# Kernel optimization log

Measured on AMD Instinct MI355X. Metric: run time of the kernel, lower is better.

## Reference

```python
import jax, jax.numpy as jnp
import numpy as np

N_NODES = 100000
N_EDGES = 1600000
D_IN = 64
D_OUT = 64


def setup_inputs() -> dict:
    key = jax.random.key(0)
    k1, k2, k3, k4, k5 = jax.random.split(key, 5)
    feat = jax.random.normal(k1, (N_NODES, D_IN), dtype=jnp.float32)
    src = jax.random.randint(k2, (N_EDGES,), 0, N_NODES, dtype=jnp.int64)
    dst = jax.random.randint(k3, (N_EDGES,), 0, N_NODES, dtype=jnp.int64)
    # Xavier-uniform init with relu gain, as in reset_parameters()
    gain = np.sqrt(2.0)
    bound = gain * np.sqrt(6.0 / (D_IN + D_OUT))
    W_self = jax.random.uniform(k4, (D_OUT, D_IN), minval=-bound, maxval=bound, dtype=jnp.float32)
    W_neigh = jax.random.uniform(k5, (D_OUT, D_IN), minval=-bound, maxval=bound, dtype=jnp.float32)
    return {"feat": feat, "src": src, "dst": dst, "W_self": W_self, "W_neigh": W_neigh}


def _spmm_mean(feat, src, dst, n_nodes):
    # Mean neighbor aggregation: for each dst node, average src features.
    gathered = feat[src]  # [E, D] irregular gather
    agg = jax.ops.segment_sum(gathered, dst, num_segments=n_nodes)  # [N, D]
    deg = jax.ops.segment_sum(jnp.ones((src.shape[0],), feat.dtype), dst, num_segments=n_nodes)
    return agg / jnp.maximum(deg, 1.0)[:, None]


def reference(feat, src, dst, W_self, W_neigh):
    neigh = _spmm_mean(feat, src, dst, feat.shape[0])  # [N, D_in]
    # rst = fc_self(feat) + fc_neigh(SpMM(feat))
    return feat @ W_self.T + neigh @ W_neigh.T
```

## Files before the change

kernel.cpp:

```cpp
#include <hip/hip_runtime.h>
#include <hip/hip_fp16.h>

#define N_NODES 100000
#define N_EDGES 1600000
#define D 64
#define ZROW 100000

#define NPB   240
#define NB    417
#define CAP   8192

#define EPB   8192
#define PBLK  ((N_EDGES + EPB - 1) / EPB)

#define W2_FF16     0u
#define W2_PACKED   12800128u
#define W2_CNT      (W2_PACKED + 4u * N_EDGES)
#define W2_OFF      (W2_CNT  + 4u * NB)
#define W2_GCUR     (W2_OFF  + 4u * NB)
#define W2_NODEOFF  (W2_GCUR + 4u * NB)
#define W2_NODECNT  (W2_NODEOFF + 4u * N_NODES)
#define W2_W16      (W2_NODECNT + 4u * N_NODES)
#define W2_NEED     (W2_W16 + 16384u)

#define W1_PACKED   0u
#define W1_CNT      (4u * N_EDGES)
#define W1_OFF      (W1_CNT  + 4u * NB)
#define W1_GCUR     (W1_OFF  + 4u * NB)
#define W1_NODEOFF  (W1_GCUR + 4u * NB)
#define W1_NODECNT  (W1_NODEOFF + 4u * N_NODES)
#define W1_NEED     (W1_NODECNT + 4u * N_NODES)

typedef __attribute__((ext_vector_type(8))) _Float16 half8;
typedef __attribute__((ext_vector_type(4))) float f32x4;

__device__ inline unsigned int h2bits(__half2 h) { return *(unsigned int*)&h; }
__device__ inline __half2 bits2h(unsigned int u) { return *(__half2*)&u; }
__device__ inline __half2 h2shfl_xor(__half2 x, int mask) {
    int i = *(int*)&x;
    i = __shfl_xor(i, mask);
    return *(__half2*)&i;
}

__global__ __launch_bounds__(256) void k_prep(
    const float* __restrict__ feat, const int* __restrict__ dst,
    const float* __restrict__ Ws, const float* __restrict__ Wn,
    unsigned int* __restrict__ ff16, int* __restrict__ cnt,
    unsigned int* __restrict__ w16)
{
    __shared__ int h[NB];
    const int bid = blockIdx.x;
    const int t   = threadIdx.x;

    if (bid < 1024) {
        const int total = N_NODES * D / 8;
        for (int i = bid * 256 + t; i < total; i += 1024 * 256) {
            const float4 x = ((const float4*)feat)[i * 2];
            const float4 y = ((const float4*)feat)[i * 2 + 1];
            uint4 o;
            o.x = h2bits(__floats2half2_rn(x.x, x.y));
            o.y = h2bits(__floats2half2_rn(x.z, x.w));
            o.z = h2bits(__floats2half2_rn(y.x, y.y));
            o.w = h2bits(__floats2half2_rn(y.z, y.w));
            ((uint4*)ff16)[i] = o;
        }
    } else if (bid < 1280) {
        for (int i = t; i < NB; i += 256) h[i] = 0;
        __syncthreads();
        for (int e = (bid - 1024) * 256 + t; e < N_EDGES; e += 256 * 256)
            atomicAdd(&h[dst[e] / NPB], 1);
        __syncthreads();
        for (int i = t; i < NB; i += 256)
            if (h[i]) atomicAdd(&cnt[i], h[i]);
    } else {
        for (int i = t; i < 2048; i += 256)
            w16[i] = h2bits(__floats2half2_rn(Ws[2 * i], Ws[2 * i + 1]));
        for (int i = t; i < 2048; i += 256)
            w16[2048 + i] = h2bits(__floats2half2_rn(Wn[2 * i], Wn[2 * i + 1]));
        if (t < 32) ff16[ZROW * 32 + t] = 0;
    }
}

__global__ __launch_bounds__(512) void k_scan(
    const int* __restrict__ cnt, int* __restrict__ off, int* __restrict__ gcur)
{
    __shared__ int lds[512];
    const int t = threadIdx.x;
    const int v = (t < NB) ? cnt[t] : 0;
    lds[t] = v;
    __syncthreads();
    for (int o = 1; o < 512; o <<= 1) {
        const int x = (t >= o) ? lds[t - o] : 0;
        __syncthreads();
        lds[t] += x;
        __syncthreads();
    }
    if (t < NB) {
        const int excl = lds[t] - v;
        off[t]  = excl;
        gcur[t] = excl;
    }
}

__global__ __launch_bounds__(1024) void k_partition(
    const int* __restrict__ src, const int* __restrict__ dst,
    int* __restrict__ gcur, int* __restrict__ packed)
{
    __shared__ int recs[EPB];
    __shared__ int cnt[NB];
    __shared__ int scn[512];
    __shared__ int pos[NB];
    __shared__ int cur[NB];
    __shared__ int dlt[NB];

    const int t  = threadIdx.x;
    const int e0 = blockIdx.x * EPB;
    const int nE = min(EPB, N_EDGES - e0);

    for (int i = t; i < NB; i += 1024) cnt[i] = 0;
    __syncthreads();

    int pk[8], bk[8];
    #pragma unroll
    for (int k = 0; k < 8; ++k) {
        const int i = t + k * 1024;
        if (i < nE) {
            const int d  = dst[e0 + i];
            const int b  = d / NPB;
            const int dl = d - b * NPB;
            pk[k] = src[e0 + i] | (dl << 17);
            bk[k] = b;
            atomicAdd(&cnt[b], 1);
        } else {
            bk[k] = -1;
        }
    }
    __syncthreads();

    if (t < 512) scn[t] = (t < NB) ? cnt[t] : 0;
    __syncthreads();
    for (int o = 1; o < 512; o <<= 1) {
        int x = 0;
        if (t < 512 && t >= o) x = scn[t - o];
        __syncthreads();
        if (t < 512) scn[t] += x;
        __syncthreads();
    }
    if (t < NB) {
        const int v    = cnt[t];
        const int excl = scn[t] - v;
        pos[t] = excl;
        cur[t] = excl;
        dlt[t] = atomicAdd(&gcur[t], v);
    }
    __syncthreads();

    #pragma unroll
    for (int k = 0; k < 8; ++k) {
        if (bk[k] >= 0) {
            const int p = atomicAdd(&cur[bk[k]], 1);
            recs[p] = pk[k];
        }
    }
    __syncthreads();

    const int w    = t >> 6;
    const int lane = t & 63;
    for (int b = w; b < NB; b += 16) {
        const int n = cnt[b];
        const int o = pos[b];
        const int g = dlt[b];
        for (int i = lane; i < n; i += 64)
            packed[g + i] = recs[o + i];
    }
}

__global__ __launch_bounds__(512) void k_sortb(
    const int* __restrict__ off, const int* __restrict__ cntg,
    int* packed,
    int* __restrict__ node_off, int* __restrict__ node_cnt)
{
    __shared__ int recs[CAP];
    __shared__ int lcnt[256];
    __shared__ int sc[256];
    __shared__ int lcur[NPB];

    const int t      = threadIdx.x;
    const int bucket = blockIdx.x;
    const int base   = off[bucket];
    int total = cntg[bucket];
    if (total > CAP) total = CAP;

    if (t < 256) lcnt[t] = 0;
    __syncthreads();

    for (int i = t; i < total; i += 512) {
        const int r = packed[base + i];
        recs[i] = r;
        atomicAdd(&lcnt[r >> 17], 1);
    }
    __syncthreads();

    if (t < 256) sc[t] = lcnt[t];
    __syncthreads();
    for (int o = 1; o < 256; o <<= 1) {
        int x = 0;
        if (t < 256 && t >= o) x = sc[t - o];
        __syncthreads();
        if (t < 256) sc[t] += x;
        __syncthreads();
    }

    if (t < NPB) {
        const int excl = sc[t] - lcnt[t];
        lcur[t] = excl;
        const int n = bucket * NPB + t;
        if (n < N_NODES) {
            node_off[n] = base + excl;
            node_cnt[n] = lcnt[t];
        }
    }
    __syncthreads();

    for (int i = t; i < total; i += 512) {
        const int r   = recs[i];
        const int pos = atomicAdd(&lcur[r >> 17], 1);
        packed[base + pos] = r & 0x1FFFF;
    }
}

__global__ __launch_bounds__(256) void k_agg_f16(
    const unsigned int* __restrict__ ff16,
    const int* __restrict__ node_off,
    const int* __restrict__ node_cnt,
    const int* __restrict__ packed,
    float* __restrict__ out)
{
    const int gtid = blockIdx.x * 256 + threadIdx.x;
    const int n    = gtid >> 6;
    const int lane = gtid & 63;
    if (n >= N_NODES) return;

    const int start = node_off[n];
    const int deg   = node_cnt[n];
    const int sub   = lane >> 3;
    const int chunk = lane & 7;

    __half2 a0 = __floats2half2_rn(0.f, 0.f);
    __half2 a1 = a0, a2 = a0, a3 = a0;

    for (int b = 0; b < deg; b += 64) {
        const int rem = min(deg - b, 64);
        int p = ZROW;
        if (lane < rem) p = packed[start + b + lane];

        const int npair = (rem + 15) >> 4;
        for (int q = 0; q < npair; ++q) {
            const int e0 = q * 16 + sub;
            const int s0 = __shfl(p, e0)     & 0x1FFFF;
            const int s1 = __shfl(p, e0 + 8) & 0x1FFFF;
            const uint4 v0 = ((const uint4*)ff16)[(size_t)s0 * 8 + chunk];
            const uint4 v1 = ((const uint4*)ff16)[(size_t)s1 * 8 + chunk];
            a0 += bits2h(v0.x);
            a1 += bits2h(v0.y);
            a2 += bits2h(v0.z);
            a3 += bits2h(v0.w);
            a0 += bits2h(v1.x);
            a1 += bits2h(v1.y);
            a2 += bits2h(v1.z);
            a3 += bits2h(v1.w);
        }
    }

    #pragma unroll
    for (int mask = 8; mask <= 32; mask <<= 1) {
        a0 += h2shfl_xor(a0, mask);
        a1 += h2shfl_xor(a1, mask);
        a2 += h2shfl_xor(a2, mask);
        a3 += h2shfl_xor(a3, mask);
    }

    if (lane < 8) {
        const float inv = 1.0f / (float)((deg > 0) ? deg : 1);
        uint4 mb;
        mb.x = h2bits(__floats2half2_rn(__low2float(a0) * inv, __high2float(a0) * inv));
        mb.y = h2bits(__floats2half2_rn(__low2float(a1) * inv, __high2float(a1) * inv));
        mb.z = h2bits(__floats2half2_rn(__low2float(a2) * inv, __high2float(a2) * inv));
        mb.w = h2bits(__floats2half2_rn(__low2float(a3) * inv, __high2float(a3) * inv));
        ((uint4*)out)[(size_t)n * 16 + lane] = mb;
    }
}

__global__ __launch_bounds__(256) void k_update_mfma(
    const unsigned int* __restrict__ ff16,
    const _Float16* __restrict__ w16,
    float* out)
{
    const int wv   = threadIdx.x >> 6;
    const int lane = threadIdx.x & 63;
    const int n0   = blockIdx.x * 64 + wv * 16;
    const int r16  = lane & 15;
    const int g    = lane >> 4;

    half8 bws[4][2], bwn[4][2];
    #pragma unroll
    for (int nt = 0; nt < 4; ++nt) {
        const int c = nt * 16 + r16;
        #pragma unroll
        for (int kt = 0; kt < 2; ++kt) {
            const int k0 = kt * 32 + g * 8;
            bws[nt][kt] = *(const half8*)(w16 + c * 64 + k0);
            bwn[nt][kt] = *(const half8*)(w16 + 4096 + c * 64 + k0);
        }
    }

    const int arow = n0 + r16;
    const int rc   = (arow < N_NODES) ? arow : (N_NODES - 1);

    f32x4 acc[4] = {{0.f,0.f,0.f,0.f}, {0.f,0.f,0.f,0.f},
                    {0.f,0.f,0.f,0.f}, {0.f,0.f,0.f,0.f}};

    #pragma unroll
    for (int kt = 0; kt < 2; ++kt) {
        const int k8 = kt * 4 + g;
        const uint4 af_u = ((const uint4*)ff16)[(size_t)rc * 8 + k8];
        const uint4 am_u = ((const uint4*)out )[(size_t)rc * 16 + k8];
        const half8 af = *(const half8*)&af_u;
        const half8 am = *(const half8*)&am_u;
        #pragma unroll
        for (int nt = 0; nt < 4; ++nt) {
            acc[nt] = __builtin_amdgcn_mfma_f32_16x16x32_f16(af, bws[nt][kt], acc[nt], 0, 0, 0);
            acc[nt] = __builtin_amdgcn_mfma_f32_16x16x32_f16(am, bwn[nt][kt], acc[nt], 0, 0, 0);
        }
    }

    #pragma unroll
    for (int nt = 0; nt < 4; ++nt) {
        #pragma unroll
        for (int r = 0; r < 4; ++r) {
            const int ro = n0 + g * 4 + r;
            if (ro < N_NODES)
                out[(size_t)ro * 64 + nt * 16 + r16] = acc[nt][r];
        }
    }
}

__global__ __launch_bounds__(256) void k_hist1(
    const int* __restrict__ dst, int* __restrict__ cnt)
{
    __shared__ int h[NB];
    const int t = threadIdx.x;
    for (int i = t; i < NB; i += 256) h[i] = 0;
    __syncthreads();
    for (int e = blockIdx.x * 256 + t; e < N_EDGES; e += gridDim.x * 256)
        atomicAdd(&h[dst[e] / NPB], 1);
    __syncthreads();
    for (int i = t; i < NB; i += 256)
        if (h[i]) atomicAdd(&cnt[i], h[i]);
}

__global__ __launch_bounds__(256) void k_aggregate(
    const float* __restrict__ feat,
    const int*   __restrict__ node_off,
    const int*   __restrict__ node_cnt,
    const int*   __restrict__ packed,
    float*       __restrict__ out)
{
    const int gtid = blockIdx.x * 256 + threadIdx.x;
    const int n    = gtid >> 6;
    const int lane = gtid & 63;
    if (n >= N_NODES) return;

    const int start = node_off[n];
    const int deg   = node_cnt[n];

    float a0 = 0.f, a1 = 0.f, a2 = 0.f, a3 = 0.f;
    for (int b = 0; b < deg; b += 64) {
        const int rem = deg - b;
        const int p   = packed[start + b + ((lane < rem) ? lane : 0)];
        const int m   = (rem < 64) ? rem : 64;
        int i = 0;
        for (; i + 4 <= m; i += 4) {
            a0 += feat[__shfl(p, i)     * D + lane];
            a1 += feat[__shfl(p, i + 1) * D + lane];
            a2 += feat[__shfl(p, i + 2) * D + lane];
            a3 += feat[__shfl(p, i + 3) * D + lane];
        }
        for (; i < m; ++i)
            a0 += feat[__shfl(p, i) * D + lane];
    }

    const float inv = 1.0f / (float)((deg > 0) ? deg : 1);
    out[n * D + lane] = ((a0 + a1) + (a2 + a3)) * inv;
}

#define RL(v, l) __int_as_float(__builtin_amdgcn_readlane(__float_as_int(v), (l)))

__global__ __launch_bounds__(256) void k_update(
    const float* __restrict__ feat,
    const float* __restrict__ Ws,
    const float* __restrict__ Wn,
    float* out)
{
    const int wid   = (blockIdx.x * 256 + threadIdx.x) >> 6;
    const int lane  = threadIdx.x & 63;
    const int nwave = (gridDim.x * 256) >> 6;

    const float4* Ws4 = (const float4*)Ws;
    const float4* Wn4 = (const float4*)Wn;
    float4 ws[16], wn[16];
    #pragma unroll
    for (int j = 0; j < 16; ++j) {
        ws[j] = Ws4[lane * 16 + j];
        wn[j] = Wn4[lane * 16 + j];
    }

    for (int n = wid; n < N_NODES; n += nwave) {
        const float f = feat[n * D + lane];
        const float a = out[n * D + lane];
        float s0 = 0.f, s1 = 0.f, m0 = 0.f, m1 = 0.f;
        #pragma unroll
        for (int j = 0; j < 16; ++j) {
            const float4 w_s = ws[j];
            const float4 w_n = wn[j];
            s0 = fmaf(RL(f, 4 * j + 0), w_s.x, s0);
            s1 = fmaf(RL(f, 4 * j + 1), w_s.y, s1);
            s0 = fmaf(RL(f, 4 * j + 2), w_s.z, s0);
            s1 = fmaf(RL(f, 4 * j + 3), w_s.w, s1);
            m0 = fmaf(RL(a, 4 * j + 0), w_n.x, m0);
            m1 = fmaf(RL(a, 4 * j + 1), w_n.y, m1);
            m0 = fmaf(RL(a, 4 * j + 2), w_n.z, m0);
            m1 = fmaf(RL(a, 4 * j + 3), w_n.w, m1);
        }
        out[n * D + lane] = (s0 + s1) + (m0 + m1);
    }
}

__global__ __launch_bounds__(256) void sage_scatter(
    const float* __restrict__ feat,
    const int*   __restrict__ src,
    const int*   __restrict__ dst,
    float*       __restrict__ agg,
    float*       __restrict__ deg)
{
    const int gtid = blockIdx.x * blockDim.x + threadIdx.x;
    const int edge = gtid >> 6;
    const int lane = gtid & 63;
    if (edge >= N_EDGES) return;
    const int s = src[edge];
    const int d = dst[edge];
    atomicAdd(&agg[d * D + lane], feat[s * D + lane]);
    if (lane == 0) atomicAdd(&deg[d], 1.0f);
}

__global__ __launch_bounds__(256) void k_update_div(
    const float* __restrict__ feat,
    const float* __restrict__ Ws,
    const float* __restrict__ Wn,
    const float* __restrict__ deg,
    float* out)
{
    const int wid   = (blockIdx.x * 256 + threadIdx.x) >> 6;
    const int lane  = threadIdx.x & 63;
    const int nwave = (gridDim.x * 256) >> 6;

    const float4* Ws4 = (const float4*)Ws;
    const float4* Wn4 = (const float4*)Wn;
    float4 ws[16], wn[16];
    #pragma unroll
    for (int j = 0; j < 16; ++j) {
        ws[j] = Ws4[lane * 16 + j];
        wn[j] = Wn4[lane * 16 + j];
    }

    for (int n = wid; n < N_NODES; n += nwave) {
        const float f = feat[n * D + lane];
        const float a = out[n * D + lane] / fmaxf(deg[n], 1.0f);
        float s0 = 0.f, s1 = 0.f, m0 = 0.f, m1 = 0.f;
        #pragma unroll
        for (int j = 0; j < 16; ++j) {
            const float4 w_s = ws[j];
            const float4 w_n = wn[j];
            s0 = fmaf(RL(f, 4 * j + 0), w_s.x, s0);
            s1 = fmaf(RL(f, 4 * j + 1), w_s.y, s1);
            s0 = fmaf(RL(f, 4 * j + 2), w_s.z, s0);
            s1 = fmaf(RL(f, 4 * j + 3), w_s.w, s1);
            m0 = fmaf(RL(a, 4 * j + 0), w_n.x, m0);
            m1 = fmaf(RL(a, 4 * j + 1), w_n.y, m1);
            m0 = fmaf(RL(a, 4 * j + 2), w_n.z, m0);
            m1 = fmaf(RL(a, 4 * j + 3), w_n.w, m1);
        }
        out[n * D + lane] = (s0 + s1) + (m0 + m1);
    }
}

extern "C" void kernel_launch(void* const* d_in, const int* in_sizes, int n_in,
                              void* d_out, int out_size, void* d_ws, size_t ws_size,
                              hipStream_t stream) {
    const float* feat = (const float*)d_in[0];
    const int*   src  = (const int*)d_in[1];
    const int*   dst  = (const int*)d_in[2];
    const float* Ws   = (const float*)d_in[3];
    const float* Wn   = (const float*)d_in[4];
    float* out = (float*)d_out;
    char*  ws  = (char*)d_ws;

    if (ws_size >= W2_NEED) {
        unsigned int* ff16 = (unsigned int*)(ws + W2_FF16);
        int* packed = (int*)(ws + W2_PACKED);
        int* cnt    = (int*)(ws + W2_CNT);
        int* off    = (int*)(ws + W2_OFF);
        int* gcur   = (int*)(ws + W2_GCUR);
        int* noff   = (int*)(ws + W2_NODEOFF);
        int* ncnt   = (int*)(ws + W2_NODECNT);
        unsigned int* w16u = (unsigned int*)(ws + W2_W16);

        hipMemsetAsync(cnt, 0, (size_t)NB * sizeof(int), stream);

        k_prep       <<<1281, 256,  0, stream>>>(feat, dst, Ws, Wn, ff16, cnt, w16u);
        k_scan       <<<1,    512,  0, stream>>>(cnt, off, gcur);
        k_partition  <<<PBLK, 1024, 0, stream>>>(src, dst, gcur, packed);
        k_sortb      <<<NB,   512,  0, stream>>>(off, cnt, packed, noff, ncnt);
        k_agg_f16    <<<(N_NODES * 64 + 255) / 256, 256, 0, stream>>>(
            ff16, noff, ncnt, packed, out);
        k_update_mfma<<<(N_NODES + 63) / 64, 256, 0, stream>>>(
            ff16, (const _Float16*)w16u, out);
    } else if (ws_size >= W1_NEED) {
        int* packed = (int*)(ws + W1_PACKED);
        int* cnt    = (int*)(ws + W1_CNT);
        int* off    = (int*)(ws + W1_OFF);
        int* gcur   = (int*)(ws + W1_GCUR);
        int* noff   = (int*)(ws + W1_NODEOFF);
        int* ncnt   = (int*)(ws + W1_NODECNT);

        hipMemsetAsync(cnt, 0, (size_t)NB * sizeof(int), stream);

        k_hist1    <<<256,  256,  0, stream>>>(dst, cnt);
        k_scan     <<<1,    512,  0, stream>>>(cnt, off, gcur);
        k_partition<<<PBLK, 1024, 0, stream>>>(src, dst, gcur, packed);
        k_sortb    <<<NB,   512,  0, stream>>>(off, cnt, packed, noff, ncnt);
        k_aggregate<<<(N_NODES * 64 + 255) / 256, 256, 0, stream>>>(
            feat, noff, ncnt, packed, out);
        k_update   <<<1024, 256,  0, stream>>>(feat, Ws, Wn, out);
    } else {
        float* deg = (float*)ws;
        hipMemsetAsync(out, 0, (size_t)N_NODES * D * sizeof(float), stream);
        hipMemsetAsync(deg, 0, (size_t)N_NODES * sizeof(float), stream);
        sage_scatter<<<(N_EDGES * 64) / 256, 256, 0, stream>>>(feat, src, dst, out, deg);
        k_update_div<<<1024, 256, 0, stream>>>(feat, Ws, Wn, deg, out);
    }
}
```

Baseline: 114.9 us.

## Use fixed-capacity buckets to drop histogram/scan and fuse aggregation with MFMA update

Replaces the histogram+scan pass with fixed-capacity per-bucket slots (bucket*CAP), so partitioning needs only atomic cursors on a zeroed counter array. The fp16 feature conversion and weight packing are folded into the partition launch as extra blocks. Aggregation and the MFMA linear update are fused into one kernel that keeps the mean rows in LDS instead of writing them to and rereading them from global memory. This cuts launches and global round trips, but the packed buffer grows, any bucket above CAP would silently drop edges, and only one wave per block does the MFMA work. The W1 fallback path is removed.

New measurement: 98.02 us. 1.17x faster.

```diff
diff --git a/kernel.cpp b/kernel.cpp
--- a/kernel.cpp
+++ b/kernel.cpp
@@ -12,24 +12,15 @@
 
 #define EPB   8192
 #define PBLK  ((N_EDGES + EPB - 1) / EPB)
-
-#define W2_FF16     0u
-#define W2_PACKED   12800128u
-#define W2_CNT      (W2_PACKED + 4u * N_EDGES)
-#define W2_OFF      (W2_CNT  + 4u * NB)
-#define W2_GCUR     (W2_OFF  + 4u * NB)
-#define W2_NODEOFF  (W2_GCUR + 4u * NB)
-#define W2_NODECNT  (W2_NODEOFF + 4u * N_NODES)
-#define W2_W16      (W2_NODECNT + 4u * N_NODES)
-#define W2_NEED     (W2_W16 + 16384u)
-
-#define W1_PACKED   0u
-#define W1_CNT      (4u * N_EDGES)
-#define W1_OFF      (W1_CNT  + 4u * NB)
-#define W1_GCUR     (W1_OFF  + 4u * NB)
-#define W1_NODEOFF  (W1_GCUR + 4u * NB)
-#define W1_NODECNT  (W1_NODEOFF + 4u * N_NODES)
-#define W1_NEED     (W1_NODECNT + 4u * N_NODES)
+#define CONVB 256
+
+#define W3_FF16     0u
+#define W3_PACKED   12800128u
+#define W3_GCUR     (W3_PACKED + 4u * NB * CAP)
+#define W3_NODEOFF  (W3_GCUR + 4u * NB)
+#define W3_NODECNT  (W3_NODEOFF + 4u * N_NODES)
+#define W3_W16      (W3_NODECNT + 4u * N_NODES)
+#define W3_NEED     (W3_W16 + 16384u)
 
 typedef __attribute__((ext_vector_type(8))) _Float16 half8;
 typedef __attribute__((ext_vector_type(4))) float f32x4;
@@ -42,68 +33,11 @@
     return *(__half2*)&i;
 }
 
-__global__ __launch_bounds__(256) void k_prep(
-    const float* __restrict__ feat, const int* __restrict__ dst,
+__global__ __launch_bounds__(1024) void k_part_conv(
+    const float* __restrict__ feat,
+    const int* __restrict__ src, const int* __restrict__ dst,
     const float* __restrict__ Ws, const float* __restrict__ Wn,
-    unsigned int* __restrict__ ff16, int* __restrict__ cnt,
-    unsigned int* __restrict__ w16)
-{
-    __shared__ int h[NB];
-    const int bid = blockIdx.x;
-    const int t   = threadIdx.x;
-
-    if (bid < 1024) {
-        const int total = N_NODES * D / 8;
-        for (int i = bid * 256 + t; i < total; i += 1024 * 256) {
-            const float4 x = ((const float4*)feat)[i * 2];
-            const float4 y = ((const float4*)feat)[i * 2 + 1];
-            uint4 o;
-            o.x = h2bits(__floats2half2_rn(x.x, x.y));
-            o.y = h2bits(__floats2half2_rn(x.z, x.w));
-            o.z = h2bits(__floats2half2_rn(y.x, y.y));
-            o.w = h2bits(__floats2half2_rn(y.z, y.w));
-            ((uint4*)ff16)[i] = o;
-        }
-    } else if (bid < 1280) {
-        for (int i = t; i < NB; i += 256) h[i] = 0;
-        __syncthreads();
-        for (int e = (bid - 1024) * 256 + t; e < N_EDGES; e += 256 * 256)
-            atomicAdd(&h[dst[e] / NPB], 1);
-        __syncthreads();
-        for (int i = t; i < NB; i += 256)
-            if (h[i]) atomicAdd(&cnt[i], h[i]);
-    } else {
-        for (int i = t; i < 2048; i += 256)
-            w16[i] = h2bits(__floats2half2_rn(Ws[2 * i], Ws[2 * i + 1]));
-        for (int i = t; i < 2048; i += 256)
-            w16[2048 + i] = h2bits(__floats2half2_rn(Wn[2 * i], Wn[2 * i + 1]));
-        if (t < 32) ff16[ZROW * 32 + t] = 0;
-    }
-}
-
-__global__ __launch_bounds__(512) void k_scan(
-    const int* __restrict__ cnt, int* __restrict__ off, int* __restrict__ gcur)
-{
-    __shared__ int lds[512];
-    const int t = threadIdx.x;
-    const int v = (t < NB) ? cnt[t] : 0;
-    lds[t] = v;
-    __syncthreads();
-    for (int o = 1; o < 512; o <<= 1) {
-        const int x = (t >= o) ? lds[t - o] : 0;
-        __syncthreads();
-        lds[t] += x;
-        __syncthreads();
-    }
-    if (t < NB) {
-        const int excl = lds[t] - v;
-        off[t]  = excl;
-        gcur[t] = excl;
-    }
-}
-
-__global__ __launch_bounds__(1024) void k_partition(
-    const int* __restrict__ src, const int* __restrict__ dst,
+    unsigned int* __restrict__ ff16, unsigned int* __restrict__ w16,
     int* __restrict__ gcur, int* __restrict__ packed)
 {
     __shared__ int recs[EPB];
@@ -113,8 +47,33 @@
     __shared__ int cur[NB];
     __shared__ int dlt[NB];
 
-    const int t  = threadIdx.x;
-    const int e0 = blockIdx.x * EPB;
+    const int bid = blockIdx.x;
+    const int t   = threadIdx.x;
+
+    if (bid >= PBLK) {
+        if (bid < PBLK + CONVB) {
+            const int total = N_NODES * D / 8;
+            for (int i = (bid - PBLK) * 1024 + t; i < total; i += CONVB * 1024) {
+                const float4 x = ((const float4*)feat)[i * 2];
+                const float4 y = ((const float4*)feat)[i * 2 + 1];
+                uint4 o;
+                o.x = h2bits(__floats2half2_rn(x.x, x.y));
+                o.y = h2bits(__floats2half2_rn(x.z, x.w));
+                o.z = h2bits(__floats2half2_rn(y.x, y.y));
+                o.w = h2bits(__floats2half2_rn(y.z, y.w));
+                ((uint4*)ff16)[i] = o;
+            }
+        } else {
+            for (int i = t; i < 2048; i += 1024) {
+                w16[i]        = h2bits(__floats2half2_rn(Ws[2 * i], Ws[2 * i + 1]));
+                w16[2048 + i] = h2bits(__floats2half2_rn(Wn[2 * i], Wn[2 * i + 1]));
+            }
+            if (t < 32) ff16[ZROW * 32 + t] = 0;
+        }
+        return;
+    }
+
+    const int e0 = bid * EPB;
     const int nE = min(EPB, N_EDGES - e0);
 
     for (int i = t; i < NB; i += 1024) cnt[i] = 0;
@@ -169,14 +128,14 @@
     for (int b = w; b < NB; b += 16) {
         const int n = cnt[b];
         const int o = pos[b];
-        const int g = dlt[b];
+        const int g = b * CAP + dlt[b];
         for (int i = lane; i < n; i += 64)
             packed[g + i] = recs[o + i];
     }
 }
 
 __global__ __launch_bounds__(512) void k_sortb(
-    const int* __restrict__ off, const int* __restrict__ cntg,
+    const int* __restrict__ gcur,
     int* packed,
     int* __restrict__ node_off, int* __restrict__ node_cnt)
 {
@@ -187,8 +146,8 @@
 
     const int t      = threadIdx.x;
     const int bucket = blockIdx.x;
-    const int base   = off[bucket];
-    int total = cntg[bucket];
+    const int base   = bucket * CAP;
+    int total = gcur[bucket];
     if (total > CAP) total = CAP;
 
     if (t < 256) lcnt[t] = 0;
@@ -229,78 +188,78 @@
     }
 }
 
-__global__ __launch_bounds__(256) void k_agg_f16(
+__global__ __launch_bounds__(1024) void k_agg_update(
     const unsigned int* __restrict__ ff16,
     const int* __restrict__ node_off,
     const int* __restrict__ node_cnt,
     const int* __restrict__ packed,
+    const _Float16* __restrict__ w16,
     float* __restrict__ out)
 {
-    const int gtid = blockIdx.x * 256 + threadIdx.x;
-    const int n    = gtid >> 6;
-    const int lane = gtid & 63;
-    if (n >= N_NODES) return;
-
-    const int start = node_off[n];
-    const int deg   = node_cnt[n];
-    const int sub   = lane >> 3;
-    const int chunk = lane & 7;
-
-    __half2 a0 = __floats2half2_rn(0.f, 0.f);
-    __half2 a1 = a0, a2 = a0, a3 = a0;
-
-    for (int b = 0; b < deg; b += 64) {
-        const int rem = min(deg - b, 64);
-        int p = ZROW;
-        if (lane < rem) p = packed[start + b + lane];
-
-        const int npair = (rem + 15) >> 4;
-        for (int q = 0; q < npair; ++q) {
-            const int e0 = q * 16 + sub;
-            const int s0 = __shfl(p, e0)     & 0x1FFFF;
-            const int s1 = __shfl(p, e0 + 8) & 0x1FFFF;
-            const uint4 v0 = ((const uint4*)ff16)[(size_t)s0 * 8 + chunk];
-            const uint4 v1 = ((const uint4*)ff16)[(size_t)s1 * 8 + chunk];
-            a0 += bits2h(v0.x);
-            a1 += bits2h(v0.y);
-            a2 += bits2h(v0.z);
-            a3 += bits2h(v0.w);
-            a0 += bits2h(v1.x);
-            a1 += bits2h(v1.y);
-            a2 += bits2h(v1.z);
-            a3 += bits2h(v1.w);
-        }
-    }
-
-    #pragma unroll
-    for (int mask = 8; mask <= 32; mask <<= 1) {
-        a0 += h2shfl_xor(a0, mask);
-        a1 += h2shfl_xor(a1, mask);
-        a2 += h2shfl_xor(a2, mask);
-        a3 += h2shfl_xor(a3, mask);
-    }
-
-    if (lane < 8) {
-        const float inv = 1.0f / (float)((deg > 0) ? deg : 1);
-        uint4 mb;
-        mb.x = h2bits(__floats2half2_rn(__low2float(a0) * inv, __high2float(a0) * inv));
-        mb.y = h2bits(__floats2half2_rn(__low2float(a1) * inv, __high2float(a1) * inv));
-        mb.z = h2bits(__floats2half2_rn(__low2float(a2) * inv, __high2float(a2) * inv));
-        mb.w = h2bits(__floats2half2_rn(__low2float(a3) * inv, __high2float(a3) * inv));
-        ((uint4*)out)[(size_t)n * 16 + lane] = mb;
-    }
-}
-
-__global__ __launch_bounds__(256) void k_update_mfma(
-    const unsigned int* __restrict__ ff16,
-    const _Float16* __restrict__ w16,
-    float* out)
-{
-    const int wv   = threadIdx.x >> 6;
-    const int lane = threadIdx.x & 63;
-    const int n0   = blockIdx.x * 64 + wv * 16;
-    const int r16  = lane & 15;
-    const int g    = lane >> 4;
+    __shared__ uint4 meanLDS[16 * 8];
+
+    const int t    = threadIdx.x;
+    const int wv   = t >> 6;
+    const int lane = t & 63;
+    const int n0   = blockIdx.x * 16;
+    const int n    = n0 + wv;
+
+    {
+        const int start = node_off[n];
+        const int deg   = node_cnt[n];
+        const int sub   = lane >> 3;
+        const int chunk = lane & 7;
+
+        __half2 a0 = __floats2half2_rn(0.f, 0.f);
+        __half2 a1 = a0, a2 = a0, a3 = a0;
+
+        for (int b = 0; b < deg; b += 64) {
+            const int rem = min(deg - b, 64);
+            int p = ZROW;
+            if (lane < rem) p = packed[start + b + lane];
+
+            const int npair = (rem + 15) >> 4;
+            for (int q = 0; q < npair; ++q) {
+                const int e0 = q * 16 + sub;
+                const int s0 = __shfl(p, e0)     & 0x1FFFF;
+                const int s1 = __shfl(p, e0 + 8) & 0x1FFFF;
+                const uint4 v0 = ((const uint4*)ff16)[(size_t)s0 * 8 + chunk];
+                const uint4 v1 = ((const uint4*)ff16)[(size_t)s1 * 8 + chunk];
+                a0 += bits2h(v0.x);
+                a1 += bits2h(v0.y);
+                a2 += bits2h(v0.z);
+                a3 += bits2h(v0.w);
+                a0 += bits2h(v1.x);
+                a1 += bits2h(v1.y);
+                a2 += bits2h(v1.z);
+                a3 += bits2h(v1.w);
+            }
+        }
+
+        #pragma unroll
+        for (int mask = 8; mask <= 32; mask <<= 1) {
+            a0 += h2shfl_xor(a0, mask);
+            a1 += h2shfl_xor(a1, mask);
+            a2 += h2shfl_xor(a2, mask);
+            a3 += h2shfl_xor(a3, mask);
+        }
+
+        if (lane < 8) {
+            const float inv = 1.0f / (float)((deg > 0) ? deg : 1);
+            uint4 mb;
+            mb.x = h2bits(__floats2half2_rn(__low2float(a0) * inv, __high2float(a0) * inv));
+            mb.y = h2bits(__floats2half2_rn(__low2float(a1) * inv, __high2float(a1) * inv));
+            mb.z = h2bits(__floats2half2_rn(__low2float(a2) * inv, __high2float(a2) * inv));
+            mb.w = h2bits(__floats2half2_rn(__low2float(a3) * inv, __high2float(a3) * inv));
+            meanLDS[wv * 8 + (lane ^ (wv & 7))] = mb;
+        }
+    }
+    __syncthreads();
+
+    if (wv != 0) return;
+
+    const int r16 = lane & 15;
+    const int g   = lane >> 4;
 
     half8 bws[4][2], bwn[4][2];
     #pragma unroll
@@ -314,17 +273,14 @@
         }
     }
 
-    const int arow = n0 + r16;
-    const int rc   = (arow < N_NODES) ? arow : (N_NODES - 1);
-
     f32x4 acc[4] = {{0.f,0.f,0.f,0.f}, {0.f,0.f,0.f,0.f},
                     {0.f,0.f,0.f,0.f}, {0.f,0.f,0.f,0.f}};
 
     #pragma unroll
     for (int kt = 0; kt < 2; ++kt) {
         const int k8 = kt * 4 + g;
-        const uint4 af_u = ((const uint4*)ff16)[(size_t)rc * 8 + k8];
-        const uint4 am_u = ((const uint4*)out )[(size_t)rc * 16 + k8];
+        const uint4 af_u = ((const uint4*)ff16)[(size_t)(n0 + r16) * 8 + k8];
+        const uint4 am_u = meanLDS[r16 * 8 + (k8 ^ (r16 & 7))];
         const half8 af = *(const half8*)&af_u;
         const half8 am = *(const half8*)&am_u;
         #pragma unroll
@@ -339,67 +295,35 @@
         #pragma unroll
         for (int r = 0; r < 4; ++r) {
             const int ro = n0 + g * 4 + r;
-            if (ro < N_NODES)
-                out[(size_t)ro * 64 + nt * 16 + r16] = acc[nt][r];
-        }
-    }
-}
-
-__global__ __launch_bounds__(256) void k_hist1(
-    const int* __restrict__ dst, int* __restrict__ cnt)
-{
-    __shared__ int h[NB];
-    const int t = threadIdx.x;
-    for (int i = t; i < NB; i += 256) h[i] = 0;
-    __syncthreads();
-    for (int e = blockIdx.x * 256 + t; e < N_EDGES; e += gridDim.x * 256)
-        atomicAdd(&h[dst[e] / NPB], 1);
-    __syncthreads();
-    for (int i = t; i < NB; i += 256)
-        if (h[i]) atomicAdd(&cnt[i], h[i]);
-}
-
-__global__ __launch_bounds__(256) void k_aggregate(
+            out[(size_t)ro * 64 + nt * 16 + r16] = acc[nt][r];
+        }
+    }
+}
+
+__global__ __launch_bounds__(256) void sage_scatter(
     const float* __restrict__ feat,
-    const int*   __restrict__ node_off,
-    const int*   __restrict__ node_cnt,
-    const int*   __restrict__ packed,
-    float*       __restrict__ out)
-{
-    const int gtid = blockIdx.x * 256 + threadIdx.x;
-    const int n    = gtid >> 6;
+    const int*   __restrict__ src,
+    const int*   __restrict__ dst,
+    float*       __restrict__ agg,
+    float*       __restrict__ deg)
+{
+    const int gtid = blockIdx.x * blockDim.x + threadIdx.x;
+    const int edge = gtid >> 6;
     const int lane = gtid & 63;
-    if (n >= N_NODES) return;
-
-    const int start = node_off[n];
-    const int deg   = node_cnt[n];
-
-    float a0 = 0.f, a1 = 0.f, a2 = 0.f, a3 = 0.f;
-    for (int b = 0; b < deg; b += 64) {
-        const int rem = deg - b;
-        const int p   = packed[start + b + ((lane < rem) ? lane : 0)];
-        const int m   = (rem < 64) ? rem : 64;
-        int i = 0;
-        for (; i + 4 <= m; i += 4) {
-            a0 += feat[__shfl(p, i)     * D + lane];
-            a1 += feat[__shfl(p, i + 1) * D + lane];
-            a2 += feat[__shfl(p, i + 2) * D + lane];
-            a3 += feat[__shfl(p, i + 3) * D + lane];
-        }
-        for (; i < m; ++i)
-            a0 += feat[__shfl(p, i) * D + lane];
-    }
-
-    const float inv = 1.0f / (float)((deg > 0) ? deg : 1);
-    out[n * D + lane] = ((a0 + a1) + (a2 + a3)) * inv;
+    if (edge >= N_EDGES) return;
+    const int s = src[edge];
+    const int d = dst[edge];
+    atomicAdd(&agg[d * D + lane], feat[s * D + lane]);
+    if (lane == 0) atomicAdd(&deg[d], 1.0f);
 }
 
 #define RL(v, l) __int_as_float(__builtin_amdgcn_readlane(__float_as_int(v), (l)))
 
-__global__ __launch_bounds__(256) void k_update(
+__global__ __launch_bounds__(256) void k_update_div(
     const float* __restrict__ feat,
     const float* __restrict__ Ws,
     const float* __restrict__ Wn,
+    const float* __restrict__ deg,
     float* out)
 {
     const int wid   = (blockIdx.x * 256 + threadIdx.x) >> 6;
@@ -417,7 +341,7 @@
 
     for (int n = wid; n < N_NODES; n += nwave) {
         const float f = feat[n * D + lane];
-        const float a = out[n * D + lane];
+        const float a = out[n * D + lane] / fmaxf(deg[n], 1.0f);
         float s0 = 0.f, s1 = 0.f, m0 = 0.f, m1 = 0.f;
         #pragma unroll
         for (int j = 0; j < 16; ++j) {
@@ -436,64 +360,6 @@
     }
 }
 
-__global__ __launch_bounds__(256) void sage_scatter(
-    const float* __restrict__ feat,
-    const int*   __restrict__ src,
-    const int*   __restrict__ dst,
-    float*       __restrict__ agg,
-    float*       __restrict__ deg)
-{
-    const int gtid = blockIdx.x * blockDim.x + threadIdx.x;
-    const int edge = gtid >> 6;
-    const int lane = gtid & 63;
-    if (edge >= N_EDGES) return;
-    const int s = src[edge];
-    const int d = dst[edge];
-    atomicAdd(&agg[d * D + lane], feat[s * D + lane]);
-    if (lane == 0) atomicAdd(&deg[d], 1.0f);
-}
-
-__global__ __launch_bounds__(256) void k_update_div(
-    const float* __restrict__ feat,
-    const float* __restrict__ Ws,
-    const float* __restrict__ Wn,
-    const float* __restrict__ deg,
-    float* out)
-{
-    const int wid   = (blockIdx.x * 256 + threadIdx.x) >> 6;
-    const int lane  = threadIdx.x & 63;
-    const int nwave = (gridDim.x * 256) >> 6;
-
-    const float4* Ws4 = (const float4*)Ws;
-    const float4* Wn4 = (const float4*)Wn;
-    float4 ws[16], wn[16];
-    #pragma unroll
-    for (int j = 0; j < 16; ++j) {
-        ws[j] = Ws4[lane * 16 + j];
-        wn[j] = Wn4[lane * 16 + j];
-    }
-
-    for (int n = wid; n < N_NODES; n += nwave) {
-        const float f = feat[n * D + lane];
-        const float a = out[n * D + lane] / fmaxf(deg[n], 1.0f);
-        float s0 = 0.f, s1 = 0.f, m0 = 0.f, m1 = 0.f;
-        #pragma unroll
-        for (int j = 0; j < 16; ++j) {
-            const float4 w_s = ws[j];
-            const float4 w_n = wn[j];
-            s0 = fmaf(RL(f, 4 * j + 0), w_s.x, s0);
-            s1 = fmaf(RL(f, 4 * j + 1), w_s.y, s1);
-            s0 = fmaf(RL(f, 4 * j + 2), w_s.z, s0);
-            s1 = fmaf(RL(f, 4 * j + 3), w_s.w, s1);
-            m0 = fmaf(RL(a, 4 * j + 0), w_n.x, m0);
-            m1 = fmaf(RL(a, 4 * j + 1), w_n.y, m1);
-            m0 = fmaf(RL(a, 4 * j + 2), w_n.z, m0);
-            m1 = fmaf(RL(a, 4 * j + 3), w_n.w, m1);
-        }
-        out[n * D + lane] = (s0 + s1) + (m0 + m1);
-    }
-}
-
 extern "C" void kernel_launch(void* const* d_in, const int* in_sizes, int n_in,
                               void* d_out, int out_size, void* d_ws, size_t ws_size,
                               hipStream_t stream) {
@@ -505,43 +371,21 @@
     float* out = (float*)d_out;
     char*  ws  = (char*)d_ws;
 
-    if (ws_size >= W2_NEED) {
-        unsigned int* ff16 = (unsigned int*)(ws + W2_FF16);
-        int* packed = (int*)(ws + W2_PACKED);
-        int* cnt    = (int*)(ws + W2_CNT);
-        int* off    = (int*)(ws + W2_OFF);
-        int* gcur   = (int*)(ws + W2_GCUR);
-        int* noff   = (int*)(ws + W2_NODEOFF);
-        int* ncnt   = (int*)(ws + W2_NODECNT);
-        unsigned int* w16u = (unsigned int*)(ws + W2_W16);
-
-        hipMemsetAsync(cnt, 0, (size_t)NB * sizeof(int), stream);
-
-        k_prep       <<<1281, 256,  0, stream>>>(feat, dst, Ws, Wn, ff16, cnt, w16u);
-        k_scan       <<<1,    512,  0, stream>>>(cnt, off, gcur);
-        k_partition  <<<PBLK, 1024, 0, stream>>>(src, dst, gcur, packed);
-        k_sortb      <<<NB,   512,  0, stream>>>(off, cnt, packed, noff, ncnt);
-        k_agg_f16    <<<(N_NODES * 64 + 255) / 256, 256, 0, stream>>>(
-            ff16, noff, ncnt, packed, out);
-        k_update_mfma<<<(N_NODES + 63) / 64, 256, 0, stream>>>(
-            ff16, (const _Float16*)w16u, out);
-    } else if (ws_size >= W1_NEED) {
-        int* packed = (int*)(ws + W1_PACKED);
-        int* cnt    = (int*)(ws + W1_CNT);
-        int* off    = (int*)(ws + W1_OFF);
-        int* gcur   = (int*)(ws + W1_GCUR);
-        int* noff   = (int*)(ws + W1_NODEOFF);
-        int* ncnt   = (int*)(ws + W1_NODECNT);
-
-        hipMemsetAsync(cnt, 0, (size_t)NB * sizeof(int), stream);
-
-        k_hist1    <<<256,  256,  0, stream>>>(dst, cnt);
-        k_scan     <<<1,    512,  0, stream>>>(cnt, off, gcur);
-        k_partition<<<PBLK, 1024, 0, stream>>>(src, dst, gcur, packed);
-        k_sortb    <<<NB,   512,  0, stream>>>(off, cnt, packed, noff, ncnt);
-        k_aggregate<<<(N_NODES * 64 + 255) / 256, 256, 0, stream>>>(
-            feat, noff, ncnt, packed, out);
-        k_update   <<<1024, 256,  0, stream>>>(feat, Ws, Wn, out);
+    if (ws_size >= W3_NEED) {
+        unsigned int* ff16 = (unsigned int*)(ws + W3_FF16);
+        int* packed = (int*)(ws + W3_PACKED);
+        int* gcur   = (int*)(ws + W3_GCUR);
+        int* noff   = (int*)(ws + W3_NODEOFF);
+        int* ncnt   = (int*)(ws + W3_NODECNT);
+        unsigned int* w16u = (unsigned int*)(ws + W3_W16);
+
+        hipMemsetAsync(gcur, 0, (size_t)NB * sizeof(int), stream);
+
+        k_part_conv <<<PBLK + CONVB + 1, 1024, 0, stream>>>(
+            feat, src, dst, Ws, Wn, ff16, w16u, gcur, packed);
+        k_sortb     <<<NB, 512, 0, stream>>>(gcur, packed, noff, ncnt);
+        k_agg_update<<<N_NODES / 16, 1024, 0, stream>>>(
+            ff16, noff, ncnt, packed, (const _Float16*)w16u, out);
     } else {
         float* deg = (float*)ws;
         hipMemsetAsync(out, 0, (size_t)N_NODES * D * sizeof(float), stream);
```
